# Kernel optimization log

Hardware: AMD Instinct MI355X
Metric: run time of the kernel (lower is better)

Reference implementation:

```python
import jax, jax.numpy as jnp
import numpy as np
from jax import lax


def _farthest_point_sample(xyz, npoint):
    """Iterative FPS, faithful to the torch loop. xyz: [B,N,3] -> centroids [B,npoint] int32."""
    B, N, _ = xyz.shape
    barycenter = jnp.mean(xyz, axis=1, keepdims=True)            # [B,1,3]
    d0 = jnp.sum((xyz - barycenter) ** 2, axis=-1)               # [B,N]
    farthest = jnp.argmax(d0, axis=1)                            # [B]
    distance = jnp.full((B, N), 1e10, dtype=xyz.dtype)
    selected = jnp.zeros((B, N), dtype=bool)
    batch_idx = jnp.arange(B)

    def step(carry, _):
        distance, selected, farthest = carry
        selected = selected.at[batch_idx, farthest].set(True)
        centroid = jnp.take_along_axis(xyz, farthest[:, None, None], axis=1)  # [B,1,3]
        d = jnp.sum((xyz - centroid) ** 2, axis=-1)              # [B,N]
        d = jnp.where(selected, 0.0, d)                          # torch: dist[selected_mask]=0
        distance = jnp.minimum(distance, d)                      # torch: distance[mask]=dist[mask]
        nxt = jnp.argmax(distance, axis=-1)
        return (distance, selected, nxt), farthest

    _, cents = lax.scan(step, (distance, selected, farthest), None, length=npoint)
    return jnp.transpose(cents)                                   # [B, npoint]


def _assign_points_to_clusters(xyz, centroids):
    """Assign every point to nearest centroid. Vectorized over batch (no python loop)."""
    cpts = jnp.take_along_axis(xyz, centroids[:, :, None], axis=1)          # [B,P,3]
    # [B,N,P] pairwise squared distances
    dist = jnp.sum((xyz[:, :, None, :] - cpts[:, None, :, :]) ** 2, axis=-1)
    return jnp.argmin(dist, axis=-1)                                         # [B,N]


def setup_inputs() -> dict:
    key = jax.random.key(0)
    B, N = 8, 100000
    xyz = jax.random.normal(key, (B, N, 3), dtype=jnp.float32)
    return {"xyz": xyz, "npoint": 64}


def reference(xyz, npoint):
    centroids = _farthest_point_sample(xyz, npoint)               # [B,P] int
    clusters = _assign_points_to_clusters(xyz, centroids)         # [B,N] int
    centroid_xyz = jnp.take_along_axis(xyz, centroids[:, :, None], axis=1)  # [B,P,3] float
    return centroid_xyz, centroids, clusters
```

## Files before the change

kernel.cpp:

```cpp
#include <hip/hip_runtime.h>

#define BATCHES 8
#define NPTS    100000
#define NPOINT  64
#define BPB     16
#define NTHREADS 1024
#define TPB     (BPB * NTHREADS)
#define KMAX    7
#define TAILN   (NPTS - (KMAX - 1) * TPB)

#define WS_BARY_OFF 0
#define WS_CNT_OFF  3072
#define WS_SLOT_OFF 4096
#define WS_CTRL_BYTES (WS_SLOT_OFF + BATCHES * NPOINT * BPB * 8)

__device__ __forceinline__ float sq3(float dx, float dy, float dz) {
    return __fadd_rn(__fadd_rn(__fmul_rn(dx, dx), __fmul_rn(dy, dy)), __fmul_rn(dz, dz));
}

__global__ __launch_bounds__(NTHREADS, 4)
void fps_kernel(const float* __restrict__ xyz, float* __restrict__ out,
                unsigned char* __restrict__ ws)
{
    double* baryPart = (double*)(ws + WS_BARY_OFF);
    unsigned int* cnt = (unsigned int*)(ws + WS_CNT_OFF);
    unsigned long long* slots = (unsigned long long*)(ws + WS_SLOT_OFF);

    const int b    = blockIdx.x >> 4;
    const int blk  = blockIdx.x & (BPB - 1);
    const int tid  = threadIdx.x;
    const int wid  = tid >> 6;
    const int lane = tid & 63;
    const int t    = blk * NTHREADS + tid;

    const float* xb = xyz + (size_t)b * NPTS * 3;

    __shared__ float centC[NPOINT][3];
    __shared__ double bred[16][3];
    __shared__ unsigned long long kred[16];
    __shared__ int s_far;

    float px[KMAX], py[KMAX], pz[KMAX], dist[KMAX];
    const int nk = (t < TAILN) ? KMAX : (KMAX - 1);

    double sx = 0.0, sy = 0.0, sz = 0.0;
    #pragma unroll
    for (int k = 0; k < KMAX; k++) {
        if (k < nk) {
            int p = t + k * TPB;
            float x = xb[p * 3 + 0], y = xb[p * 3 + 1], z = xb[p * 3 + 2];
            px[k] = x; py[k] = y; pz[k] = z; dist[k] = 1e10f;
            sx += (double)x; sy += (double)y; sz += (double)z;
        }
    }
    for (int off = 32; off > 0; off >>= 1) {
        sx += __shfl_down(sx, off); sy += __shfl_down(sy, off); sz += __shfl_down(sz, off);
    }
    if (lane == 0) { bred[wid][0] = sx; bred[wid][1] = sy; bred[wid][2] = sz; }
    __syncthreads();
    __shared__ float s_bc[3];
    if (tid == 0) {
        double ax = 0, ay = 0, az = 0;
        for (int w = 0; w < 16; w++) { ax += bred[w][0]; ay += bred[w][1]; az += bred[w][2]; }
        double* dst = baryPart + ((size_t)b * BPB + blk) * 3;
        dst[0] = ax; dst[1] = ay; dst[2] = az;
        __hip_atomic_fetch_add(&cnt[b], 1u, __ATOMIC_ACQ_REL, __HIP_MEMORY_SCOPE_AGENT);
        while (__hip_atomic_load(&cnt[b], __ATOMIC_ACQUIRE, __HIP_MEMORY_SCOPE_AGENT) < BPB)
            __builtin_amdgcn_s_sleep(2);
        double mx = 0, my = 0, mz = 0;
        for (int q = 0; q < BPB; q++) {
            const double* s2 = baryPart + ((size_t)b * BPB + q) * 3;
            mx += s2[0]; my += s2[1]; mz += s2[2];
        }
        s_bc[0] = (float)(mx / (double)NPTS);
        s_bc[1] = (float)(my / (double)NPTS);
        s_bc[2] = (float)(mz / (double)NPTS);
    }
    __syncthreads();
    const float bx = s_bc[0], by = s_bc[1], bz = s_bc[2];

    unsigned long long key = 0;
    #pragma unroll
    for (int k = 0; k < KMAX; k++) {
        if (k < nk) {
            int p = t + k * TPB;
            float d = sq3(__fsub_rn(px[k], bx), __fsub_rn(py[k], by), __fsub_rn(pz[k], bz));
            unsigned long long kk = (((unsigned long long)__float_as_uint(d)) << 32)
                                    | (unsigned)(0xFFFFFFFFu - (unsigned)p);
            if (kk > key) key = kk;
        }
    }
    #define EXCHANGE(ROUND)                                                                  \
    {                                                                                        \
        for (int off = 32; off > 0; off >>= 1) {                                             \
            unsigned long long o = __shfl_down(key, off); if (o > key) key = o;              \
        }                                                                                    \
        if (lane == 0) kred[wid] = key;                                                      \
        __syncthreads();                                                                     \
        if (wid == 0) {                                                                      \
            unsigned long long v = (lane < 16) ? kred[lane] : 0ull;                          \
            for (int m = 8; m > 0; m >>= 1) {                                                \
                unsigned long long o = __shfl_xor(v, m, 16); if (o > v) v = o;               \
            }                                                                                \
            unsigned long long* row = &slots[((size_t)b * NPOINT + (ROUND)) * BPB];          \
            if (lane == 0)                                                                   \
                __hip_atomic_store(&row[blk], v, __ATOMIC_RELAXED, __HIP_MEMORY_SCOPE_AGENT);\
            unsigned long long w = 0;                                                        \
            if (lane < BPB) {                                                                \
                while ((w = __hip_atomic_load(&row[lane], __ATOMIC_RELAXED,                  \
                                              __HIP_MEMORY_SCOPE_AGENT)) == 0ull)           \
                    __builtin_amdgcn_s_sleep(1);                                             \
            }                                                                                \
            for (int m = 8; m > 0; m >>= 1) {                                                \
                unsigned long long o = __shfl_xor(w, m, 16); if (o > w) w = o;               \
            }                                                                                \
            if (lane == 0)                                                                   \
                s_far = (int)(0xFFFFFFFFu - (unsigned)(w & 0xFFFFFFFFull));                  \
        }                                                                                    \
    }
    EXCHANGE(0)

    for (int i = 0; i < NPOINT; i++) {
        __syncthreads();
        const int f = s_far;
        const float cx = xb[f * 3 + 0], cy = xb[f * 3 + 1], cz = xb[f * 3 + 2];
        if (tid == 0) {
            centC[i][0] = cx; centC[i][1] = cy; centC[i][2] = cz;
            if (blk == 0) {
                out[((size_t)b * NPOINT + i) * 3 + 0] = cx;
                out[((size_t)b * NPOINT + i) * 3 + 1] = cy;
                out[((size_t)b * NPOINT + i) * 3 + 2] = cz;
                out[(size_t)BATCHES * NPOINT * 3 + b * NPOINT + i] = (float)f;
            }
        }
        if (i == NPOINT - 1) break;

        key = 0;
        #pragma unroll
        for (int k = 0; k < KMAX; k++) {
            if (k < nk) {
                int p = t + k * TPB;
                float d = sq3(__fsub_rn(px[k], cx), __fsub_rn(py[k], cy), __fsub_rn(pz[k], cz));
                float nd = (p == f) ? 0.0f : fminf(dist[k], d);
                dist[k] = nd;
                unsigned long long kk = (((unsigned long long)__float_as_uint(nd)) << 32)
                                        | (unsigned)(0xFFFFFFFFu - (unsigned)p);
                if (kk > key) key = kk;
            }
        }
        EXCHANGE(i + 1)
    }
    __syncthreads();

    float* outClust = out + (size_t)BATCHES * NPOINT * 3 + (size_t)BATCHES * NPOINT;
    float bestd[KMAX]; int besti[KMAX];
    #pragma unroll
    for (int k = 0; k < KMAX; k++) { bestd[k] = 3.4e38f; besti[k] = 0; }
    for (int j = 0; j < NPOINT; j++) {
        float cx = centC[j][0], cy = centC[j][1], cz = centC[j][2];
        #pragma unroll
        for (int k = 0; k < KMAX; k++) {
            if (k < nk) {
                float d = sq3(__fsub_rn(px[k], cx), __fsub_rn(py[k], cy), __fsub_rn(pz[k], cz));
                if (d < bestd[k]) { bestd[k] = d; besti[k] = j; }
            }
        }
    }
    #pragma unroll
    for (int k = 0; k < KMAX; k++)
        if (k < nk) outClust[(size_t)b * NPTS + t + k * TPB] = (float)besti[k];
}

extern "C" void kernel_launch(void* const* d_in, const int* in_sizes, int n_in,
                              void* d_out, int out_size, void* d_ws, size_t ws_size,
                              hipStream_t stream) {
    const float* xyz = (const float*)d_in[0];
    float* out = (float*)d_out;
    hipMemsetAsync(d_ws, 0, WS_CTRL_BYTES, stream);
    fps_kernel<<<dim3(BATCHES * BPB), dim3(NTHREADS), 0, stream>>>(
        xyz, out, (unsigned char*)d_ws);
}
```

Measured before the change: 186.3 us.

## Replace per-round block barriers with LDS flag-based wave signaling in FPS loop

Removes the two __syncthreads per FPS round. Waves now publish their per-wave argmax into double-buffered LDS slots with release stores, and wave 0 polls them, reduces, exchanges across blocks and posts the winner in a round-tagged LDS flag that all waves spin on. The aim is to cut block-wide barrier cost on the 64-round serial critical path. In exchange it adds LDS spin-waiting with s_sleep, and correctness depends on the parity buffering and the zero-reset of candidate slots.

```diff
diff --git a/kernel.cpp b/kernel.cpp
--- a/kernel.cpp
+++ b/kernel.cpp
@@ -37,11 +37,15 @@
 
     __shared__ float centC[NPOINT][3];
     __shared__ double bred[16][3];
-    __shared__ unsigned long long kred[16];
-    __shared__ int s_far;
+    __shared__ unsigned long long kcand[2][16];
+    __shared__ unsigned int wflag[2];
+    __shared__ float s_bc[3];
 
     float px[KMAX], py[KMAX], pz[KMAX], dist[KMAX];
     const int nk = (t < TAILN) ? KMAX : (KMAX - 1);
+
+    if (tid < 32) kcand[tid >> 4][tid & 15] = 0ull;
+    if (tid == 32) { wflag[0] = 0u; wflag[1] = 0u; }
 
     double sx = 0.0, sy = 0.0, sz = 0.0;
     #pragma unroll
@@ -58,7 +62,6 @@
     }
     if (lane == 0) { bred[wid][0] = sx; bred[wid][1] = sy; bred[wid][2] = sz; }
     __syncthreads();
-    __shared__ float s_bc[3];
     if (tid == 0) {
         double ax = 0, ay = 0, az = 0;
         for (int w = 0; w < 16; w++) { ax += bred[w][0]; ay += bred[w][1]; az += bred[w][2]; }
@@ -90,51 +93,67 @@
             if (kk > key) key = kk;
         }
     }
-    #define EXCHANGE(ROUND)                                                                  \
-    {                                                                                        \
-        for (int off = 32; off > 0; off >>= 1) {                                             \
-            unsigned long long o = __shfl_down(key, off); if (o > key) key = o;              \
-        }                                                                                    \
-        if (lane == 0) kred[wid] = key;                                                      \
-        __syncthreads();                                                                     \
-        if (wid == 0) {                                                                      \
-            unsigned long long v = (lane < 16) ? kred[lane] : 0ull;                          \
-            for (int m = 8; m > 0; m >>= 1) {                                                \
-                unsigned long long o = __shfl_xor(v, m, 16); if (o > v) v = o;               \
-            }                                                                                \
-            unsigned long long* row = &slots[((size_t)b * NPOINT + (ROUND)) * BPB];          \
-            if (lane == 0)                                                                   \
-                __hip_atomic_store(&row[blk], v, __ATOMIC_RELAXED, __HIP_MEMORY_SCOPE_AGENT);\
-            unsigned long long w = 0;                                                        \
-            if (lane < BPB) {                                                                \
-                while ((w = __hip_atomic_load(&row[lane], __ATOMIC_RELAXED,                  \
-                                              __HIP_MEMORY_SCOPE_AGENT)) == 0ull)           \
-                    __builtin_amdgcn_s_sleep(1);                                             \
-            }                                                                                \
-            for (int m = 8; m > 0; m >>= 1) {                                                \
-                unsigned long long o = __shfl_xor(w, m, 16); if (o > w) w = o;               \
-            }                                                                                \
-            if (lane == 0)                                                                   \
-                s_far = (int)(0xFFFFFFFFu - (unsigned)(w & 0xFFFFFFFFull));                  \
-        }                                                                                    \
-    }
-    EXCHANGE(0)
-
-    for (int i = 0; i < NPOINT; i++) {
-        __syncthreads();
-        const int f = s_far;
+
+    for (int e = 0; e < NPOINT; e++) {
+        const int par = e & 1;
+        for (int off = 32; off > 0; off >>= 1) {
+            unsigned long long o = __shfl_down(key, off); if (o > key) key = o;
+        }
+        if (lane == 0)
+            __hip_atomic_store(&kcand[par][wid], key, __ATOMIC_RELEASE, __HIP_MEMORY_SCOPE_WORKGROUP);
+
+        if (wid == 0) {
+            unsigned long long v = 0;
+            if (lane < 16) {
+                unsigned long long kk;
+                while ((kk = __hip_atomic_load(&kcand[par][lane], __ATOMIC_ACQUIRE,
+                                               __HIP_MEMORY_SCOPE_WORKGROUP)) == 0ull)
+                    __builtin_amdgcn_s_sleep(1);
+                __hip_atomic_store(&kcand[par][lane], 0ull, __ATOMIC_RELAXED,
+                                   __HIP_MEMORY_SCOPE_WORKGROUP);
+                v = kk;
+            }
+            for (int m = 8; m > 0; m >>= 1) {
+                unsigned long long o = __shfl_xor(v, m, 16); if (o > v) v = o;
+            }
+            unsigned long long* row = &slots[((size_t)b * NPOINT + e) * BPB];
+            if (lane == 0)
+                __hip_atomic_store(&row[blk], v, __ATOMIC_RELAXED, __HIP_MEMORY_SCOPE_AGENT);
+            unsigned long long w = 0;
+            if (lane < BPB) {
+                while ((w = __hip_atomic_load(&row[lane], __ATOMIC_RELAXED,
+                                              __HIP_MEMORY_SCOPE_AGENT)) == 0ull)
+                    __builtin_amdgcn_s_sleep(1);
+            }
+            for (int m = 8; m > 0; m >>= 1) {
+                unsigned long long o = __shfl_xor(w, m, 16); if (o > w) w = o;
+            }
+            if (lane == 0) {
+                unsigned f = 0xFFFFFFFFu - (unsigned)(w & 0xFFFFFFFFull);
+                __hip_atomic_store(&wflag[par], (((unsigned)(e + 1)) << 18) | f,
+                                   __ATOMIC_RELEASE, __HIP_MEMORY_SCOPE_WORKGROUP);
+            }
+        }
+
+        unsigned vfl;
+        while (((vfl = __hip_atomic_load(&wflag[par], __ATOMIC_ACQUIRE,
+                                         __HIP_MEMORY_SCOPE_WORKGROUP)) >> 18) != (unsigned)(e + 1))
+            __builtin_amdgcn_s_sleep(1);
+        const int f = (int)(vfl & 0x3FFFFu);
+
+        if (wid == 1 && lane == 0) {
+            float cx = xb[f * 3 + 0], cy = xb[f * 3 + 1], cz = xb[f * 3 + 2];
+            centC[e][0] = cx; centC[e][1] = cy; centC[e][2] = cz;
+            if (blk == 0) {
+                out[((size_t)b * NPOINT + e) * 3 + 0] = cx;
+                out[((size_t)b * NPOINT + e) * 3 + 1] = cy;
+                out[((size_t)b * NPOINT + e) * 3 + 2] = cz;
+                out[(size_t)BATCHES * NPOINT * 3 + b * NPOINT + e] = (float)f;
+            }
+        }
+        if (e == NPOINT - 1) break;
+
         const float cx = xb[f * 3 + 0], cy = xb[f * 3 + 1], cz = xb[f * 3 + 2];
-        if (tid == 0) {
-            centC[i][0] = cx; centC[i][1] = cy; centC[i][2] = cz;
-            if (blk == 0) {
-                out[((size_t)b * NPOINT + i) * 3 + 0] = cx;
-                out[((size_t)b * NPOINT + i) * 3 + 1] = cy;
-                out[((size_t)b * NPOINT + i) * 3 + 2] = cz;
-                out[(size_t)BATCHES * NPOINT * 3 + b * NPOINT + i] = (float)f;
-            }
-        }
-        if (i == NPOINT - 1) break;
-
         key = 0;
         #pragma unroll
         for (int k = 0; k < KMAX; k++) {
@@ -148,7 +167,6 @@
                 if (kk > key) key = kk;
             }
         }
-        EXCHANGE(i + 1)
     }
     __syncthreads();
 
```

Measured after the change: 199.0 us. +6.8%, slower.
